# Optimization experiments

Measured on AMD Instinct MI355X. Metric: run time of the kernel, lower is better.

The kernel has to match this reference:

```python
import jax, jax.numpy as jnp
import numpy as np

H, D, BS = 32, 128, 64          # num_heads, head_dim, gate block_size
GATE_DIM = 64
GATE_TEMP = 2.0                 # _GATE_TARGET_TEMPERATURE
CLAMP_MIN, CLAMP_MAX = -50.0, 50.0


def _rotate_half(x):
    x1, x2 = jnp.split(x, 2, axis=-1)
    return jnp.concatenate([-x2, x1], axis=-1)


def setup_inputs() -> dict:
    key = jax.random.key(0)
    ks = jax.random.split(key, 8)
    B, S, E = 1, 2048, 4096
    hidden_states = jax.random.normal(ks[0], (B, S, E), jnp.float32) * 0.02
    # standard RoPE tables, [B, S, D]
    inv_freq = 1.0 / (10000.0 ** (jnp.arange(0, D, 2, dtype=jnp.float32) / D))
    freqs = jnp.arange(S, dtype=jnp.float32)[:, None] * inv_freq[None, :]
    emb = jnp.concatenate([freqs, freqs], axis=-1)
    cos = jnp.broadcast_to(jnp.cos(emb)[None], (B, S, D)).astype(jnp.float32)
    sin = jnp.broadcast_to(jnp.sin(emb)[None], (B, S, D)).astype(jnp.float32)
    Wq = jax.random.normal(ks[1], (E, E), jnp.float32) * 0.02
    Wk = jax.random.normal(ks[2], (E, E), jnp.float32) * 0.02
    Wv = jax.random.normal(ks[3], (E, E), jnp.float32) * 0.02
    Wo = jax.random.normal(ks[4], (E, E), jnp.float32) * 0.02
    Wg_q = jax.random.normal(ks[5], (GATE_DIM, D), jnp.float32) * 0.05
    Wg_k = jax.random.normal(ks[6], (GATE_DIM, D), jnp.float32) * 0.05
    return {"hidden_states": hidden_states, "cos": cos, "sin": sin,
            "Wq": Wq, "Wk": Wk, "Wv": Wv, "Wo": Wo,
            "Wg_q": Wg_q, "Wg_k": Wg_k}


def reference(hidden_states, cos, sin, Wq, Wk, Wv, Wo, Wg_q, Wg_k):
    B, S, E = hidden_states.shape
    scale = np.float32(1.0 / np.sqrt(D))

    # ---- base attention (training path: full dense attention w/ scores) ----
    q = (hidden_states @ Wq.T).reshape(B, S, H, D).transpose(0, 2, 1, 3)  # [B,H,S,D]
    k = (hidden_states @ Wk.T).reshape(B, S, H, D).transpose(0, 2, 1, 3)
    v = (hidden_states @ Wv.T).reshape(B, S, H, D).transpose(0, 2, 1, 3)

    # _apply_rotary_pos_emb: cos/sin are 3D [B,S,D] -> unsqueeze head dim
    c, s = cos[:, None], sin[:, None]
    q = q * c + _rotate_half(q) * s
    k = k * c + _rotate_half(k) * s

    scores = jnp.einsum('bhqd,bhkd->bhqk', q, k) * scale  # [B,H,S,S]
    causal = jnp.tril(jnp.ones((S, S), dtype=bool))
    scores = jnp.where(causal, scores, -jnp.inf)
    attn = jax.nn.softmax(scores, axis=-1)
    ctx = jnp.einsum('bhqk,bhkd->bhqd', attn, v)
    attn_output = ctx.transpose(0, 2, 1, 3).reshape(B, S, E) @ Wo.T

    # ---- _compute_gate_target: blockwise maxpool -> clamp -> tempered softmax ----
    NB = S // BS  # S divisible by BS, so the -inf padding branch is a no-op
    block_max = scores.reshape(B, H, NB, BS, NB, BS).max(axis=(3, 5))  # [B,H,NB,NB]
    finite = jnp.isfinite(block_max)
    block_max = jnp.where(finite, jnp.clip(block_max, CLAMP_MIN, CLAMP_MAX), block_max)
    gate_target = jax.nn.softmax(
        block_max.reshape(B, H, NB * NB) / GATE_TEMP, axis=-1
    ).reshape(B, H, NB, NB)

    # ---- AttnGate prediction: mean-pooled block Q/K -> low-rank block logits ----
    qb = q.reshape(B, H, NB, BS, D).mean(axis=3)  # [B,H,NB,D]
    kb = k.reshape(B, H, NB, BS, D).mean(axis=3)
    gq = jnp.einsum('bhnd,gd->bhng', qb, Wg_q)
    gk = jnp.einsum('bhnd,gd->bhng', kb, Wg_k)
    glogits = jnp.einsum('bhqg,bhkg->bhqk', gq, gk) * np.float32(1.0 / np.sqrt(GATE_DIM))
    bmask = jnp.tril(jnp.ones((NB, NB), dtype=bool))  # block-causal
    glogits = jnp.where(bmask, glogits, -jnp.inf)
    gate_pred = jax.nn.softmax(
        glogits.reshape(B, H, NB * NB), axis=-1
    ).reshape(B, H, NB, NB)

    return attn_output, gate_pred, gate_target
```

## Files before the change

### kernel.cpp

```cpp
#include <hip/hip_runtime.h>
#include <stdint.h>

#define S_LEN 2048
#define EMB   4096
#define NHEAD 32
#define DHEAD 128
#define NBLK  32
#define GDIM  64

typedef float  f32x4  __attribute__((ext_vector_type(4)));
typedef __bf16 bf16x8 __attribute__((ext_vector_type(8)));
typedef unsigned short u16;

__device__ __forceinline__ u16 f2bf(float f) {
  uint32_t u = __float_as_uint(f);
  u += 0x7fffu + ((u >> 16) & 1u);
  return (u16)(u >> 16);
}
__device__ __forceinline__ float bf2f(u16 u) {
  return __uint_as_float(((uint32_t)u) << 16);
}

__device__ __forceinline__ void ld_lds16(const u16* g, u16* l) {
  __builtin_amdgcn_global_load_lds((const __attribute__((address_space(1))) void*)g,
                                   (__attribute__((address_space(3))) void*)l, 16, 0, 0);
}

__global__ void conv_f32_bf16(const float* __restrict__ in, u16* __restrict__ out, int n4) {
  int i = blockIdx.x * 256 + threadIdx.x;
  if (i >= n4) return;
  float4 v = ((const float4*)in)[i];
  ushort4 o;
  o.x = f2bf(v.x); o.y = f2bf(v.y); o.z = f2bf(v.z); o.w = f2bf(v.w);
  ((ushort4*)out)[i] = o;
}

__global__ void conv3_f32_bf16(const float* __restrict__ a, const float* __restrict__ b,
                               const float* __restrict__ c, u16* __restrict__ oa,
                               u16* __restrict__ ob, u16* __restrict__ oc, int n4) {
  int i = blockIdx.x * 256 + threadIdx.x;
  if (i >= n4) return;
  const float* in = (blockIdx.y == 0) ? a : (blockIdx.y == 1) ? b : c;
  u16* out = (blockIdx.y == 0) ? oa : (blockIdx.y == 1) ? ob : oc;
  float4 v = ((const float4*)in)[i];
  ushort4 o;
  o.x = f2bf(v.x); o.y = f2bf(v.y); o.z = f2bf(v.z); o.w = f2bf(v.w);
  ((ushort4*)out)[i] = o;
}

__global__ void __launch_bounds__(512, 2) qkv_gemm_256(
    const u16* __restrict__ A, const u16* __restrict__ Bq, const u16* __restrict__ Bk,
    const u16* __restrict__ Bv, u16* __restrict__ outq, u16* __restrict__ outk,
    u16* __restrict__ outvt, const float* __restrict__ cosp, const float* __restrict__ sinp)
{
  extern __shared__ u16 lds[];

  const int tid  = threadIdx.x;
  const int w    = tid >> 6;
  const int lane = tid & 63;
  const int r    = lane & 15;
  const int qd   = lane >> 4;
  const int wr   = w >> 2;
  const int wc   = w & 3;
  const int hh   = wc >> 1;

  const int bid   = blockIdx.x;
  const int nb    = (bid & 7) * 48 + (bid >> 3);
  const int xx    = nb % 48;
  const int which = xx >> 4;
  const int nt    = xx & 15;
  const int m0    = (nb / 48) * 256;
  const int n0    = nt * 256;
  const int K     = EMB;
  const u16* Bm = (which == 0) ? Bq : (which == 1) ? Bk : Bv;

  const int swz0 = (qd ^ (r & 7)) * 8;
  const int swz1 = ((4 + qd) ^ (r & 7)) * 8;
  const int rowbaseA = (wr * 64 + r) * 64;
  const int rowbaseB = (hh * 64 + (wc & 1) * 16 + r) * 64;

  const int srw = tid >> 3;
  const int sgs = ((tid & 7) ^ (srw & 7)) * 8;
  const u16* pA0 = A + (size_t)(m0 + srw) * K + sgs;
  const int fm = ((srw >> 5) & 1) * 64 + (srw & 31);
  const u16* pB0 = Bm + (size_t)(n0 + fm) * K + sgs;

  f32x4 acc[8][4];
#pragma unroll
  for (int mi = 0; mi < 8; ++mi)
#pragma unroll
    for (int ni = 0; ni < 4; ++ni) acc[mi][ni] = (f32x4){0.f, 0.f, 0.f, 0.f};

  auto stA = [&](int tt, int half) {
    u16* d = lds + ((tt & 1) * 2 + half) * 8192 + w * 512;
    const u16* g = pA0 + (size_t)(half * 128) * K + tt * 64;
    ld_lds16(g, d);
    ld_lds16(g + (size_t)64 * K, d + 4096);
  };
  auto stB = [&](int tt, int half) {
    u16* d = lds + 32768 + ((tt & 1) * 2 + half) * 8192 + w * 512;
    const u16* g = pB0 + (size_t)(half * 32) * K + tt * 64;
    ld_lds16(g, d);
    ld_lds16(g + (size_t)128 * K, d + 4096);
  };

  stA(0, 0); stB(0, 0); stB(0, 1); stA(0, 1);
  asm volatile("s_waitcnt vmcnt(0)" ::: "memory");
  __builtin_amdgcn_s_barrier();

  for (int t = 0; t < 64; ++t) {
    const u16* bufA = lds + (t & 1) * 16384;
    const u16* bufB = lds + 32768 + (t & 1) * 16384;
    bf16x8 aF[4][2], bLo[2][2], bHi[2][2];

    {
      const u16* ab = bufA + rowbaseA;
      const u16* bb = bufB + rowbaseB;
#pragma unroll
      for (int mi = 0; mi < 4; ++mi) {
        aF[mi][0] = *(const bf16x8*)(ab + mi * 1024 + swz0);
        aF[mi][1] = *(const bf16x8*)(ab + mi * 1024 + swz1);
      }
#pragma unroll
      for (int ni = 0; ni < 2; ++ni) {
        bLo[ni][0] = *(const bf16x8*)(bb + ni * 2048 + swz0);
        bLo[ni][1] = *(const bf16x8*)(bb + ni * 2048 + swz1);
      }
    }
    if (t < 63) stA(t + 1, 0);
    __builtin_amdgcn_s_barrier();
    asm volatile("s_waitcnt lgkmcnt(0)" ::: "memory");
    __builtin_amdgcn_sched_barrier(0);
    __builtin_amdgcn_s_setprio(1);
#pragma unroll
    for (int mi = 0; mi < 4; ++mi)
#pragma unroll
      for (int ni = 0; ni < 2; ++ni) {
        acc[mi][ni] = __builtin_amdgcn_mfma_f32_16x16x32_bf16(aF[mi][0], bLo[ni][0], acc[mi][ni], 0, 0, 0);
        acc[mi][ni] = __builtin_amdgcn_mfma_f32_16x16x32_bf16(aF[mi][1], bLo[ni][1], acc[mi][ni], 0, 0, 0);
      }
    __builtin_amdgcn_s_setprio(0);
    if (t < 63) asm volatile("s_waitcnt vmcnt(4)" ::: "memory");
    else        asm volatile("s_waitcnt vmcnt(2)" ::: "memory");
    __builtin_amdgcn_s_barrier();

    {
      const u16* bb = bufB + 8192 + rowbaseB;
#pragma unroll
      for (int ni = 0; ni < 2; ++ni) {
        bHi[ni][0] = *(const bf16x8*)(bb + ni * 2048 + swz0);
        bHi[ni][1] = *(const bf16x8*)(bb + ni * 2048 + swz1);
      }
    }
    if (t < 63) stB(t + 1, 0);
    __builtin_amdgcn_s_barrier();
    asm volatile("s_waitcnt lgkmcnt(0)" ::: "memory");
    __builtin_amdgcn_sched_barrier(0);
    __builtin_amdgcn_s_setprio(1);
#pragma unroll
    for (int mi = 0; mi < 4; ++mi)
#pragma unroll
      for (int ni = 0; ni < 2; ++ni) {
        acc[mi][ni + 2] = __builtin_amdgcn_mfma_f32_16x16x32_bf16(aF[mi][0], bHi[ni][0], acc[mi][ni + 2], 0, 0, 0);
        acc[mi][ni + 2] = __builtin_amdgcn_mfma_f32_16x16x32_bf16(aF[mi][1], bHi[ni][1], acc[mi][ni + 2], 0, 0, 0);
      }
    __builtin_amdgcn_s_setprio(0);
    if (t < 63) asm volatile("s_waitcnt vmcnt(4)" ::: "memory");
    else        asm volatile("s_waitcnt vmcnt(0)" ::: "memory");
    __builtin_amdgcn_s_barrier();

    {
      const u16* ab = bufA + 8192 + rowbaseA;
#pragma unroll
      for (int mi = 0; mi < 4; ++mi) {
        aF[mi][0] = *(const bf16x8*)(ab + mi * 1024 + swz0);
        aF[mi][1] = *(const bf16x8*)(ab + mi * 1024 + swz1);
      }
    }
    if (t < 63) stB(t + 1, 1);
    __builtin_amdgcn_s_barrier();
    asm volatile("s_waitcnt lgkmcnt(0)" ::: "memory");
    __builtin_amdgcn_sched_barrier(0);
    __builtin_amdgcn_s_setprio(1);
#pragma unroll
    for (int mi = 0; mi < 4; ++mi)
#pragma unroll
      for (int ni = 0; ni < 2; ++ni) {
        acc[mi + 4][ni + 2] = __builtin_amdgcn_mfma_f32_16x16x32_bf16(aF[mi][0], bHi[ni][0], acc[mi + 4][ni + 2], 0, 0, 0);
        acc[mi + 4][ni + 2] = __builtin_amdgcn_mfma_f32_16x16x32_bf16(aF[mi][1], bHi[ni][1], acc[mi + 4][ni + 2], 0, 0, 0);
      }
    __builtin_amdgcn_s_setprio(0);
    __builtin_amdgcn_s_barrier();

    if (t < 63) stA(t + 1, 1);
    __builtin_amdgcn_s_barrier();
    __builtin_amdgcn_s_setprio(1);
#pragma unroll
    for (int mi = 0; mi < 4; ++mi)
#pragma unroll
      for (int ni = 0; ni < 2; ++ni) {
        acc[mi + 4][ni] = __builtin_amdgcn_mfma_f32_16x16x32_bf16(aF[mi][0], bLo[ni][0], acc[mi + 4][ni], 0, 0, 0);
        acc[mi + 4][ni] = __builtin_amdgcn_mfma_f32_16x16x32_bf16(aF[mi][1], bLo[ni][1], acc[mi + 4][ni], 0, 0, 0);
      }
    __builtin_amdgcn_s_setprio(0);
    if (t < 63) asm volatile("s_waitcnt vmcnt(4)" ::: "memory");
    __builtin_amdgcn_s_barrier();
  }

  if (which < 2) {
    u16* out = which ? outk : outq;
    const int hh_out = 2 * nt + hh;
#pragma unroll
    for (int mi = 0; mi < 8; ++mi) {
      const int rbase = m0 + (mi >> 2) * 128 + wr * 64 + (mi & 3) * 16 + qd * 4;
#pragma unroll
      for (int pp = 0; pp < 2; ++pp) {
        const int dlo = pp * 32 + (wc & 1) * 16 + r;
#pragma unroll
        for (int rg = 0; rg < 4; ++rg) {
          int srow = rbase + rg;
          float c = cosp[srow * DHEAD + dlo];
          float s = sinp[srow * DHEAD + dlo];
          float lo = acc[mi][pp * 2 + 0][rg], hi = acc[mi][pp * 2 + 1][rg];
          size_t base = ((size_t)hh_out * S_LEN + srow) * DHEAD;
          out[base + dlo]      = f2bf(lo * c - hi * s);
          out[base + dlo + 64] = f2bf(hi * c + lo * s);
        }
      }
    }
  } else {
    u16* lT = lds;
#pragma unroll
    for (int ch = 0; ch < 2; ++ch) {
      __syncthreads();
#pragma unroll
      for (int mq = 0; mq < 4; ++mq) {
        const int mi = ch * 4 + mq;
        const int lr = wr * 64 + mq * 16 + qd * 4;
#pragma unroll
        for (int ni = 0; ni < 4; ++ni) {
          const int col = hh * 128 + (ni >> 1) * 32 + (wc & 1) * 16 + (ni & 1) * 64 + r;
#pragma unroll
          for (int rg = 0; rg < 4; ++rg)
            lT[col * 136 + lr + rg] = f2bf(acc[mi][ni][rg]);
        }
      }
      __syncthreads();
      const int c = tid >> 1, sh = (tid & 1) * 64;
      const int hh2 = 2 * nt + (c >> 7), d = c & 127;
      size_t obase = ((size_t)hh2 * DHEAD + d) * S_LEN + m0 + ch * 128 + sh;
#pragma unroll
      for (int i8 = 0; i8 < 8; ++i8) {
        uint4 v = *(const uint4*)&lT[c * 136 + sh + i8 * 8];
        *(uint4*)&outvt[obase + i8 * 8] = v;
      }
    }
  }
}

__global__ void __launch_bounds__(256, 2) gemm_out(
    const u16* __restrict__ A, const u16* __restrict__ B, float* __restrict__ out)
{
  __shared__ u16 lA[128 * 32];
  __shared__ u16 lB[128 * 32];
  const int tid = threadIdx.x;
  const int w = tid >> 6, lane = tid & 63;
  const int r = lane & 15, qd = lane >> 4;
  const int bid = blockIdx.x + (blockIdx.y << 5);
  const int nbx = (bid & 7) * 64 + (bid >> 3);
  const int m0 = (nbx >> 5) * 128, n0 = (nbx & 31) * 128;
  const int K = EMB;

  f32x4 acc[2][8];
#pragma unroll
  for (int mi = 0; mi < 2; ++mi)
#pragma unroll
    for (int ni = 0; ni < 8; ++ni) acc[mi][ni] = (f32x4){0.f, 0.f, 0.f, 0.f};

  const u16* Ab = A + (size_t)(m0 + w * 16 + (lane >> 2)) * K + (lane & 3) * 8;
  const u16* Bb = B + (size_t)(n0 + w * 16 + (lane >> 2)) * K + (lane & 3) * 8;
  u16* lAb = &lA[(w * 16) * 32];
  u16* lBb = &lB[(w * 16) * 32];

  for (int k0 = 0; k0 < K; k0 += 32) {
    __syncthreads();
    ld_lds16(Ab + k0, lAb);
    ld_lds16(Ab + (size_t)64 * K + k0, lAb + 64 * 32);
    ld_lds16(Bb + k0, lBb);
    ld_lds16(Bb + (size_t)64 * K + k0, lBb + 64 * 32);
    __syncthreads();
    bf16x8 af0 = *(const bf16x8*)&lA[(w * 32 + r) * 32 + qd * 8];
    bf16x8 af1 = *(const bf16x8*)&lA[(w * 32 + 16 + r) * 32 + qd * 8];
#pragma unroll
    for (int ni = 0; ni < 8; ++ni) {
      bf16x8 bf = *(const bf16x8*)&lB[(ni * 16 + r) * 32 + qd * 8];
      acc[0][ni] = __builtin_amdgcn_mfma_f32_16x16x32_bf16(af0, bf, acc[0][ni], 0, 0, 0);
      acc[1][ni] = __builtin_amdgcn_mfma_f32_16x16x32_bf16(af1, bf, acc[1][ni], 0, 0, 0);
    }
  }
#pragma unroll
  for (int mi = 0; mi < 2; ++mi)
#pragma unroll
    for (int ni = 0; ni < 8; ++ni)
#pragma unroll
      for (int rg = 0; rg < 4; ++rg) {
        int srow = m0 + w * 32 + mi * 16 + qd * 4 + rg;
        out[(size_t)srow * EMB + n0 + ni * 16 + r] = acc[mi][ni][rg];
      }
}

__global__ void __launch_bounds__(256, 2) attn_fwd(
    const u16* __restrict__ qg, const u16* __restrict__ kg, const u16* __restrict__ vtg,
    u16* __restrict__ ctx, float* __restrict__ bmax)
{
  __shared__ u16 lK[64 * 132];
  __shared__ u16 lV[128 * 76];
  __shared__ u16 lP[64 * 76];
  __shared__ float lBM[4 * NBLK];

  const int tid = threadIdx.x;
  const int w = tid >> 6, lane = tid & 63;
  const int r = lane & 15, qd = lane >> 4;
  const int h = blockIdx.y;
  const u16* ksrc = kg + (size_t)h * S_LEN * DHEAD;
  const u16* vsrc = vtg + (size_t)h * DHEAD * S_LEN;
  const float scale = 0.08838834764831845f;

  for (int qsel = 0; qsel < 2; ++qsel) {
    const int qb = qsel ? (31 - (int)blockIdx.x) : (int)blockIdx.x;

    bf16x8 qf[4];
    {
      const u16* qp = qg + ((size_t)h * S_LEN + qb * 64 + w * 16 + r) * DHEAD + qd * 8;
#pragma unroll
      for (int ki = 0; ki < 4; ++ki) qf[ki] = *(const bf16x8*)(qp + ki * 32);
    }

    f32x4 o[8];
#pragma unroll
    for (int dt = 0; dt < 8; ++dt) o[dt] = (f32x4){0.f, 0.f, 0.f, 0.f};
    float m_run[4], l_run[4];
#pragma unroll
    for (int rg = 0; rg < 4; ++rg) { m_run[rg] = -__builtin_inff(); l_run[rg] = 0.f; }

    for (int kb = 0; kb <= qb; ++kb) {
      __syncthreads();
#pragma unroll
      for (int i = 0; i < 4; ++i) {
        int c = tid + 256 * i;
        int row = c >> 4, col = (c & 15) * 8;
        *(uint4*)&lK[row * 132 + col] = *(const uint4*)(ksrc + (size_t)(kb * 64 + row) * DHEAD + col);
      }
#pragma unroll
      for (int i = 0; i < 4; ++i) {
        int c = tid + 256 * i;
        int row = c >> 3, col = (c & 7) * 8;
        *(uint4*)&lV[row * 76 + col] = *(const uint4*)(vsrc + (size_t)row * S_LEN + kb * 64 + col);
      }
      __syncthreads();

      f32x4 sf[4];
#pragma unroll
      for (int nt = 0; nt < 4; ++nt) sf[nt] = (f32x4){0.f, 0.f, 0.f, 0.f};
#pragma unroll
      for (int ki = 0; ki < 4; ++ki)
#pragma unroll
        for (int nt = 0; nt < 4; ++nt) {
          bf16x8 bf = *(const bf16x8*)&lK[(nt * 16 + r) * 132 + ki * 32 + qd * 8];
          sf[nt] = __builtin_amdgcn_mfma_f32_16x16x32_bf16(qf[ki], bf, sf[nt], 0, 0, 0);
        }

      float rmax[4];
#pragma unroll
      for (int rg = 0; rg < 4; ++rg) rmax[rg] = -__builtin_inff();
#pragma unroll
      for (int nt = 0; nt < 4; ++nt)
#pragma unroll
        for (int rg = 0; rg < 4; ++rg) {
          float s = sf[nt][rg] * scale;
          if (kb == qb) {
            int col = nt * 16 + r, row = w * 16 + qd * 4 + rg;
            if (col > row) s = -__builtin_inff();
          }
          sf[nt][rg] = s;
          rmax[rg] = fmaxf(rmax[rg], s);
        }
#pragma unroll
      for (int rg = 0; rg < 4; ++rg) {
        float v = rmax[rg];
        v = fmaxf(v, __shfl_xor(v, 1));
        v = fmaxf(v, __shfl_xor(v, 2));
        v = fmaxf(v, __shfl_xor(v, 4));
        v = fmaxf(v, __shfl_xor(v, 8));
        rmax[rg] = v;
      }
      {
        float v = fmaxf(fmaxf(rmax[0], rmax[1]), fmaxf(rmax[2], rmax[3]));
        v = fmaxf(v, __shfl_xor(v, 16));
        v = fmaxf(v, __shfl_xor(v, 32));
        if (lane == 0) lBM[w * NBLK + kb] = v;
      }

      float alpha[4], rsum[4];
#pragma unroll
      for (int rg = 0; rg < 4; ++rg) {
        float mn = fmaxf(m_run[rg], rmax[rg]);
        alpha[rg] = __expf(m_run[rg] - mn);
        m_run[rg] = mn;
        rsum[rg] = 0.f;
      }
#pragma unroll
      for (int nt = 0; nt < 4; ++nt)
#pragma unroll
        for (int rg = 0; rg < 4; ++rg) {
          float p = __expf(sf[nt][rg] - m_run[rg]);
          sf[nt][rg] = p;
          rsum[rg] += p;
        }
#pragma unroll
      for (int rg = 0; rg < 4; ++rg) {
        float v = rsum[rg];
        v += __shfl_xor(v, 1);
        v += __shfl_xor(v, 2);
        v += __shfl_xor(v, 4);
        v += __shfl_xor(v, 8);
        l_run[rg] = l_run[rg] * alpha[rg] + v;
      }
#pragma unroll
      for (int nt = 0; nt < 4; ++nt)
#pragma unroll
        for (int rg = 0; rg < 4; ++rg)
          lP[(w * 16 + qd * 4 + rg) * 76 + nt * 16 + r] = f2bf(sf[nt][rg]);
#pragma unroll
      for (int dt = 0; dt < 8; ++dt)
#pragma unroll
        for (int rg = 0; rg < 4; ++rg) o[dt][rg] *= alpha[rg];
      bf16x8 pa0 = *(const bf16x8*)&lP[(w * 16 + r) * 76 + qd * 8];
      bf16x8 pa1 = *(const bf16x8*)&lP[(w * 16 + r) * 76 + 32 + qd * 8];
#pragma unroll
      for (int dt = 0; dt < 8; ++dt) {
        bf16x8 bv0 = *(const bf16x8*)&lV[(dt * 16 + r) * 76 + qd * 8];
        bf16x8 bv1 = *(const bf16x8*)&lV[(dt * 16 + r) * 76 + 32 + qd * 8];
        o[dt] = __builtin_amdgcn_mfma_f32_16x16x32_bf16(pa0, bv0, o[dt], 0, 0, 0);
        o[dt] = __builtin_amdgcn_mfma_f32_16x16x32_bf16(pa1, bv1, o[dt], 0, 0, 0);
      }
    }

    float inv[4];
#pragma unroll
    for (int rg = 0; rg < 4; ++rg) inv[rg] = 1.f / l_run[rg];
#pragma unroll
    for (int dt = 0; dt < 8; ++dt)
#pragma unroll
      for (int rg = 0; rg < 4; ++rg) {
        int srow = qb * 64 + w * 16 + qd * 4 + rg;
        ctx[(size_t)srow * EMB + h * DHEAD + dt * 16 + r] = f2bf(o[dt][rg] * inv[rg]);
      }
    __syncthreads();
    if (tid <= qb) {
      float v = fmaxf(fmaxf(lBM[0 * NBLK + tid], lBM[1 * NBLK + tid]),
                      fmaxf(lBM[2 * NBLK + tid], lBM[3 * NBLK + tid]));
      bmax[((size_t)h * NBLK + qb) * NBLK + tid] = v;
    }
  }
}

__global__ void bmean2(const u16* __restrict__ q, const u16* __restrict__ k,
                       float* __restrict__ qo, float* __restrict__ ko) {
  int nb = blockIdx.x, h = blockIdx.y, t = threadIdx.x;
  const u16* x = blockIdx.z ? k : q;
  float* out = blockIdx.z ? ko : qo;
  const u16* p = x + ((size_t)h * S_LEN + nb * 64) * DHEAD + t * 2;
  float s0 = 0.f, s1 = 0.f;
#pragma unroll 8
  for (int i = 0; i < 64; ++i) {
    uint32_t v = *(const uint32_t*)(p + (size_t)i * DHEAD);
    s0 += bf2f((u16)v);
    s1 += bf2f((u16)(v >> 16));
  }
  float2 rr = {s0 * (1.f / 64.f), s1 * (1.f / 64.f)};
  *(float2*)&out[((size_t)h * NBLK + nb) * DHEAD + t * 2] = rr;
}

__global__ void __launch_bounds__(256) gate_kernel(
    const float* __restrict__ qm, const float* __restrict__ km,
    const float* __restrict__ Wgq, const float* __restrict__ Wgk,
    const float* __restrict__ bmx, float* __restrict__ gpred, float* __restrict__ gtgt)
{
  __shared__ float gq[NBLK * GDIM], gk[NBLK * GDIM];
  __shared__ float red[256];
  const int h = blockIdx.x, tid = threadIdx.x;

  for (int i = 0; i < 8; ++i) {
    int e = tid + 256 * i;
    int n = e >> 6, g = e & 63;
    const float* qrow = qm + ((size_t)h * NBLK + n) * DHEAD;
    const float* krow = km + ((size_t)h * NBLK + n) * DHEAD;
    const float* wq = Wgq + g * DHEAD;
    const float* wk = Wgk + g * DHEAD;
    float s1 = 0.f, s2 = 0.f;
    for (int d = 0; d < DHEAD; ++d) { s1 += qrow[d] * wq[d]; s2 += krow[d] * wk[d]; }
    gq[e] = s1; gk[e] = s2;
  }
  __syncthreads();

  float gl[4];
  for (int i = 0; i < 4; ++i) {
    int idx = tid + 256 * i;
    int qn = idx >> 5, kn = idx & 31;
    if (kn <= qn) {
      float s = 0.f;
      for (int g = 0; g < GDIM; ++g) s += gq[qn * GDIM + g] * gk[kn * GDIM + g];
      gl[i] = s * 0.125f;
    } else gl[i] = -__builtin_inff();
  }
  float mx = fmaxf(fmaxf(gl[0], gl[1]), fmaxf(gl[2], gl[3]));
  red[tid] = mx; __syncthreads();
  for (int st = 128; st > 0; st >>= 1) { if (tid < st) red[tid] = fmaxf(red[tid], red[tid + st]); __syncthreads(); }
  float gmax = red[0]; __syncthreads();
  float ex[4], lsum = 0.f;
  for (int i = 0; i < 4; ++i) { ex[i] = __expf(gl[i] - gmax); lsum += ex[i]; }
  red[tid] = lsum; __syncthreads();
  for (int st = 128; st > 0; st >>= 1) { if (tid < st) red[tid] += red[tid + st]; __syncthreads(); }
  float invs = 1.f / red[0]; __syncthreads();
  for (int i = 0; i < 4; ++i) gpred[(size_t)h * 1024 + tid + 256 * i] = ex[i] * invs;

  float tl[4];
  for (int i = 0; i < 4; ++i) {
    int idx = tid + 256 * i;
    int qn = idx >> 5, kn = idx & 31;
    tl[i] = (kn <= qn) ? fminf(fmaxf(bmx[(size_t)h * 1024 + idx], -50.f), 50.f) * 0.5f
                       : -__builtin_inff();
  }
  float mx2 = fmaxf(fmaxf(tl[0], tl[1]), fmaxf(tl[2], tl[3]));
  red[tid] = mx2; __syncthreads();
  for (int st = 128; st > 0; st >>= 1) { if (tid < st) red[tid] = fmaxf(red[tid], red[tid + st]); __syncthreads(); }
  float tmax = red[0]; __syncthreads();
  float ex2[4], ls2 = 0.f;
  for (int i = 0; i < 4; ++i) { ex2[i] = __expf(tl[i] - tmax); ls2 += ex2[i]; }
  red[tid] = ls2; __syncthreads();
  for (int st = 128; st > 0; st >>= 1) { if (tid < st) red[tid] += red[tid + st]; __syncthreads(); }
  float inv2 = 1.f / red[0];
  for (int i = 0; i < 4; ++i) gtgt[(size_t)h * 1024 + tid + 256 * i] = ex2[i] * inv2;
}

extern "C" void kernel_launch(void* const* d_in, const int* in_sizes, int n_in,
                              void* d_out, int out_size, void* d_ws, size_t ws_size,
                              hipStream_t stream) {
  const float* hidden = (const float*)d_in[0];
  const float* cosp   = (const float*)d_in[1];
  const float* sinp   = (const float*)d_in[2];
  const float* Wq     = (const float*)d_in[3];
  const float* Wk     = (const float*)d_in[4];
  const float* Wv     = (const float*)d_in[5];
  const float* Wo     = (const float*)d_in[6];
  const float* Wgq    = (const float*)d_in[7];
  const float* Wgk    = (const float*)d_in[8];

  char* ws = (char*)d_ws;
  u16* wqb = (u16*)ws;
  u16* wkb = (u16*)(ws + 33554432);
  u16* hid = (u16*)(ws + 67108864);
  u16* qbf = (u16*)(ws + 83886080);
  u16* kbf = (u16*)(ws + 100663296);
  u16* vtb = (u16*)(ws + 117440512);
  float* bmx = (float*)(ws + 33554432);
  float* qmn = (float*)(ws + 33554432 + 131072);
  float* kmn = (float*)(ws + 33554432 + 655360);
  u16* ctx = hid;
  u16* wvb = (u16*)d_out;

  float* attn_out = (float*)d_out;
  float* gpred = attn_out + (size_t)S_LEN * EMB;
  float* gtgt  = gpred + NHEAD * NBLK * NBLK;

  conv3_f32_bf16<<<dim3(16384, 3), 256, 0, stream>>>(Wq, Wk, Wv, wqb, wkb, wvb, 4194304);
  conv_f32_bf16<<<8192, 256, 0, stream>>>(hidden, hid, 2097152);

  static bool attr_set = false;
  if (!attr_set) {
    (void)hipFuncSetAttribute((const void*)qkv_gemm_256,
                              hipFuncAttributeMaxDynamicSharedMemorySize, 131072);
    attr_set = true;
  }
  qkv_gemm_256<<<dim3(384), 512, 131072, stream>>>(hid, wqb, wkb, wvb, qbf, kbf, vtb, cosp, sinp);

  conv_f32_bf16<<<16384, 256, 0, stream>>>(Wo, wqb, 4194304);

  attn_fwd<<<dim3(16, NHEAD), 256, 0, stream>>>(qbf, kbf, vtb, ctx, bmx);

  bmean2<<<dim3(NBLK, NHEAD, 2), 128, 0, stream>>>(qbf, kbf, qmn, kmn);
  gate_kernel<<<NHEAD, 256, 0, stream>>>(qmn, kmn, Wgq, Wgk, bmx, gpred, gtgt);

  gemm_out<<<dim3(32, 16), 256, 0, stream>>>(ctx, wqb, attn_out);
}
```

Baseline: 789.5 us.

## Read K/V directly from global in attention and drop block swizzles in GEMMs

```diff
diff --git a/kernel.cpp b/kernel.cpp
--- a/kernel.cpp
+++ b/kernel.cpp
@@ -64,12 +64,9 @@
   const int wc   = w & 3;
   const int hh   = wc >> 1;
 
-  const int bid   = blockIdx.x;
-  const int nb    = (bid & 7) * 48 + (bid >> 3);
-  const int xx    = nb % 48;
-  const int which = xx >> 4;
-  const int nt    = xx & 15;
-  const int m0    = (nb / 48) * 256;
+  const int which = blockIdx.x >> 4;
+  const int nt    = blockIdx.x & 15;
+  const int m0    = blockIdx.y * 256;
   const int n0    = nt * 256;
   const int K     = EMB;
   const u16* Bm = (which == 0) ? Bq : (which == 1) ? Bk : Bv;
@@ -266,9 +263,7 @@
   const int tid = threadIdx.x;
   const int w = tid >> 6, lane = tid & 63;
   const int r = lane & 15, qd = lane >> 4;
-  const int bid = blockIdx.x + (blockIdx.y << 5);
-  const int nbx = (bid & 7) * 64 + (bid >> 3);
-  const int m0 = (nbx >> 5) * 128, n0 = (nbx & 31) * 128;
+  const int m0 = blockIdx.y * 128, n0 = blockIdx.x * 128;
   const int K = EMB;
 
   f32x4 acc[2][8];
@@ -309,12 +304,10 @@
       }
 }
 
-__global__ void __launch_bounds__(256, 2) attn_fwd(
+__global__ void __launch_bounds__(256, 3) attn_fwd(
     const u16* __restrict__ qg, const u16* __restrict__ kg, const u16* __restrict__ vtg,
     u16* __restrict__ ctx, float* __restrict__ bmax)
 {
-  __shared__ u16 lK[64 * 132];
-  __shared__ u16 lV[128 * 76];
   __shared__ u16 lP[64 * 76];
   __shared__ float lBM[4 * NBLK];
 
@@ -344,20 +337,8 @@
     for (int rg = 0; rg < 4; ++rg) { m_run[rg] = -__builtin_inff(); l_run[rg] = 0.f; }
 
     for (int kb = 0; kb <= qb; ++kb) {
-      __syncthreads();
-#pragma unroll
-      for (int i = 0; i < 4; ++i) {
-        int c = tid + 256 * i;
-        int row = c >> 4, col = (c & 15) * 8;
-        *(uint4*)&lK[row * 132 + col] = *(const uint4*)(ksrc + (size_t)(kb * 64 + row) * DHEAD + col);
-      }
-#pragma unroll
-      for (int i = 0; i < 4; ++i) {
-        int c = tid + 256 * i;
-        int row = c >> 3, col = (c & 7) * 8;
-        *(uint4*)&lV[row * 76 + col] = *(const uint4*)(vsrc + (size_t)row * S_LEN + kb * 64 + col);
-      }
-      __syncthreads();
+      const u16* kbase = ksrc + (size_t)(kb * 64) * DHEAD;
+      const u16* vbase = vsrc + kb * 64;
 
       f32x4 sf[4];
 #pragma unroll
@@ -366,7 +347,7 @@
       for (int ki = 0; ki < 4; ++ki)
 #pragma unroll
         for (int nt = 0; nt < 4; ++nt) {
-          bf16x8 bf = *(const bf16x8*)&lK[(nt * 16 + r) * 132 + ki * 32 + qd * 8];
+          bf16x8 bf = *(const bf16x8*)(kbase + (size_t)(nt * 16 + r) * DHEAD + ki * 32 + qd * 8);
           sf[nt] = __builtin_amdgcn_mfma_f32_16x16x32_bf16(qf[ki], bf, sf[nt], 0, 0, 0);
         }
 
@@ -439,8 +420,8 @@
       bf16x8 pa1 = *(const bf16x8*)&lP[(w * 16 + r) * 76 + 32 + qd * 8];
 #pragma unroll
       for (int dt = 0; dt < 8; ++dt) {
-        bf16x8 bv0 = *(const bf16x8*)&lV[(dt * 16 + r) * 76 + qd * 8];
-        bf16x8 bv1 = *(const bf16x8*)&lV[(dt * 16 + r) * 76 + 32 + qd * 8];
+        bf16x8 bv0 = *(const bf16x8*)(vbase + (size_t)(dt * 16 + r) * S_LEN + qd * 8);
+        bf16x8 bv1 = *(const bf16x8*)(vbase + (size_t)(dt * 16 + r) * S_LEN + 32 + qd * 8);
         o[dt] = __builtin_amdgcn_mfma_f32_16x16x32_bf16(pa0, bv0, o[dt], 0, 0, 0);
         o[dt] = __builtin_amdgcn_mfma_f32_16x16x32_bf16(pa1, bv1, o[dt], 0, 0, 0);
       }
@@ -462,6 +443,7 @@
                       fmaxf(lBM[2 * NBLK + tid], lBM[3 * NBLK + tid]));
       bmax[((size_t)h * NBLK + qb) * NBLK + tid] = v;
     }
+    __syncthreads();
   }
 }
 
@@ -583,7 +565,7 @@
                               hipFuncAttributeMaxDynamicSharedMemorySize, 131072);
     attr_set = true;
   }
-  qkv_gemm_256<<<dim3(384), 512, 131072, stream>>>(hid, wqb, wkb, wvb, qbf, kbf, vtb, cosp, sinp);
+  qkv_gemm_256<<<dim3(48, 8), 512, 131072, stream>>>(hid, wqb, wkb, wvb, qbf, kbf, vtb, cosp, sinp);
 
   conv_f32_bf16<<<16384, 256, 0, stream>>>(Wo, wqb, 4194304);
 
```

After: 945.2 us. 1.2x slower.
